# Optimization experiments

Measured on AMD Instinct MI355X. Metric: run time of the kernel, lower is better.

Reference implementation:

```python
import jax, jax.numpy as jnp
import numpy as np


def _lga_pass(x, filters, radius):
    # x: [N, C, H, W]; filters: [N, (2r+1)^2, H, W]
    # out[n,c,h,w] = sum_{i,j in [-r,r]} filters[n,(i+r)*(2r+1)+(j+r),h,w] * x[n,c,h+i,w+j]
    N, C, H, W = x.shape
    k = 2 * radius + 1
    xp = jnp.pad(x, ((0, 0), (0, 0), (radius, radius), (radius, radius)))
    out = jnp.zeros_like(x)
    idx = 0
    for i in range(k):  # fixed small kernel loop (25 taps), accumulates without materializing [N,C,H,W,25]
        for j in range(k):
            out = out + filters[:, idx:idx + 1] * xp[:, :, i:i + H, j:j + W]
            idx += 1
    return out


def setup_inputs() -> dict:
    key = jax.random.key(0)
    k1, k2 = jax.random.split(key)
    input1 = jax.random.normal(k1, (2, 64, 256, 512), dtype=jnp.float32)
    input2 = jax.random.uniform(k2, (2, 25, 256, 512), dtype=jnp.float32)
    return {"input1": input1, "input2": input2, "radius": 2}


def reference(input1, input2, radius):
    # LGA applied twice with the same per-pixel filters (Lga2Function.forward)
    temp = _lga_pass(input1, input2, radius)
    out = _lga_pass(temp, input2, radius)
    return out
```

## Files before the change

### kernel.cpp

```cpp
#include <hip/hip_runtime.h>
#include <hip/hip_fp16.h>


typedef __fp16 h2v __attribute__((ext_vector_type(2)));

#define OH 12
#define OW 60
#define USH 40

__device__ __forceinline__ unsigned pkh(float a, float b) {
    union { h2v h; unsigned u; } c;
    c.h = __builtin_amdgcn_cvt_pkrtz(a, b);
    return c.u;
}

#define M(ac, fv, xv, sf, sx) \
    asm("v_fma_mix_f32 %0, %1, %2, %0 op_sel:[" #sf "," #sx ",0] op_sel_hi:[1,1,0]" \
        : "+v"(ac) : "v"(fv), "v"(xv));

#define ROWM(T, w0, w1, w2, w3) \
  M(a0,frA[T+0],w0,0,0) M(a1,frA[T+0],w0,1,1) M(a2,frB[T+0],w1,0,0) M(a3,frB[T+0],w1,1,1) \
  M(a0,frA[T+1],w0,0,1) M(a1,frA[T+1],w1,1,0) M(a2,frB[T+1],w1,0,1) M(a3,frB[T+1],w2,1,0) \
  M(a0,frA[T+2],w1,0,0) M(a1,frA[T+2],w1,1,1) M(a2,frB[T+2],w2,0,0) M(a3,frB[T+2],w2,1,1) \
  M(a0,frA[T+3],w1,0,1) M(a1,frA[T+3],w2,1,0) M(a2,frB[T+3],w2,0,1) M(a3,frB[T+3],w3,1,0) \
  M(a0,frA[T+4],w2,0,0) M(a1,frA[T+4],w2,1,1) M(a2,frB[T+4],w3,0,0) M(a3,frB[T+4],w3,1,1)

#define LBAR() { asm volatile("s_waitcnt lgkmcnt(0)" ::: "memory"); \
                 __builtin_amdgcn_s_barrier(); asm volatile("" ::: "memory"); }

__global__ __launch_bounds__(256)
void lga2_fused(const float* __restrict__ x, const float* __restrict__ f,
                float* __restrict__ out, int N, int C, int H, int W, int CPB) {
    const int tid = threadIdx.x;
    const int r = tid >> 4;
    const int s = tid & 15;
    const int oh0 = blockIdx.y * OH;
    const int ow0 = blockIdx.x * OW;
    const int CG = C / CPB;
    const int n  = blockIdx.z / CG;
    const int c0 = (blockIdx.z % CG) * CPB;
    const int HW = H * W;

    __shared__ unsigned sxU[2][20 * USH];
    __shared__ unsigned stU[16 * USH];

    if (tid < 32) {
        int row = tid & 15;
        stU[row * USH + ((tid & 16) ? 33 : 0)] = 0u;
    }

    const int gh_f = oh0 - 2 + r;
    const int gwb  = ow0 - 2 + 4 * s;
    const bool rowok = (gh_f >= 0) && (gh_f < H);
    const bool p0ok = rowok && (gwb >= 0) && (gwb + 1 < W);
    const bool p1ok = rowok && (gwb + 3 < W);
    const float* fb = f + (size_t)(n * 25) * HW + (size_t)(rowok ? gh_f : 0) * W;

    unsigned frA[25], frB[25];
    #pragma unroll
    for (int t = 0; t < 25; ++t) {
        float2 v01 = p0ok ? *(const float2*)(fb + (size_t)t * HW + gwb)
                          : make_float2(0.f, 0.f);
        float2 v23 = p1ok ? *(const float2*)(fb + (size_t)t * HW + gwb + 2)
                          : make_float2(0.f, 0.f);
        frA[t] = pkh(v01.x, v01.y);
        frB[t] = pkh(v23.x, v23.y);
        if ((t % 5) == 4) __builtin_amdgcn_sched_barrier(0);
    }
    #pragma unroll
    for (int t = 0; t < 25; ++t)
        asm volatile("" : "+v"(frA[t]), "+v"(frB[t]));

    const int i1 = tid + 256;
    const bool has1 = (tid < 340 - 256);
    const int row0 = tid / 17, v0 = tid - row0 * 17;
    const int row1 = i1 / 17,  v1 = i1 - row1 * 17;
    const int g0h = oh0 - 4 + row0, g0c = ow0 - 4 + 4 * v0;
    const int g1h = oh0 - 4 + row1, g1c = ow0 - 4 + 4 * v1;
    const bool ok0 = (g0h >= 0) && (g0h < H) && (g0c >= 0) && (g0c + 3 < W);
    const bool ok1 = has1 && (g1h >= 0) && (g1h < H) && (g1c >= 0) && (g1c + 3 < W);
    const int off0 = ok0 ? (g0h * W + g0c) : 0;
    const int off1 = ok1 ? (g1h * W + g1c) : 0;
    const int l0u = row0 * USH + 2 * v0;
    const int l1u = row1 * USH + 2 * v1;

    const float4 z4 = make_float4(0.f, 0.f, 0.f, 0.f);
    const float* xc = x + (size_t)(n * C + c0) * HW;

    {
        float4 p = ok0 ? *(const float4*)(xc + off0) : z4;
        *(uint2*)&sxU[0][l0u] = make_uint2(pkh(p.x, p.y), pkh(p.z, p.w));
        if (has1) {
            float4 q = ok1 ? *(const float4*)(xc + off1) : z4;
            *(uint2*)&sxU[0][l1u] = make_uint2(pkh(q.x, q.y), pkh(q.z, q.w));
        }
    }
    __syncthreads();

    const bool prow = (r >= 2) && (r <= 13) && (gh_f < H);
    const int rc = (r < 2) ? 2 : ((r > 13) ? 13 : r);
    float* op = out + ((size_t)(n * C + c0) * H + gh_f) * W + gwb;

    int cur = 0;
    for (int cc = 0; cc < CPB; ++cc) {
        float4 nx0 = z4, nx1 = z4;
        const bool pf = (cc + 1 < CPB);
        if (pf) {
            const float* xn = xc + (size_t)(cc + 1) * HW;
            if (ok0) nx0 = *(const float4*)(xn + off0);
            if (ok1) nx1 = *(const float4*)(xn + off1);
        }

        float a0 = 0.f, a1 = 0.f, a2 = 0.f, a3 = 0.f;
        {
            const unsigned* sxp = sxU[cur];
            #pragma unroll
            for (int i = 0; i < 5; ++i) {
                const int b = (r + i) * USH + 2 * s;
                uint2 lo = *(const uint2*)&sxp[b];
                uint2 hi = *(const uint2*)&sxp[b + 2];
                ROWM(5 * i, lo.x, lo.y, hi.x, hi.y)
            }
        }
        stU[r * USH + 1 + 2 * s] = pkh(a0, a1);
        stU[r * USH + 2 + 2 * s] = pkh(a2, a3);
        LBAR();

        a0 = 0.f; a1 = 0.f; a2 = 0.f; a3 = 0.f;
        #pragma unroll
        for (int i = 0; i < 5; ++i) {
            const int b = (rc - 2 + i) * USH + 2 * s;
            uint2 lo = *(const uint2*)&stU[b];
            uint2 hi = *(const uint2*)&stU[b + 2];
            ROWM(5 * i, lo.x, lo.y, hi.x, hi.y)
        }
        if (prow) {
            if (s >= 1 && gwb + 1 < W)  *(float2*)op       = make_float2(a0, a1);
            if (s <= 14 && gwb + 3 < W) *(float2*)(op + 2) = make_float2(a2, a3);
        }

        if (pf) {
            *(uint2*)&sxU[cur ^ 1][l0u] = make_uint2(pkh(nx0.x, nx0.y), pkh(nx0.z, nx0.w));
            if (has1)
                *(uint2*)&sxU[cur ^ 1][l1u] = make_uint2(pkh(nx1.x, nx1.y), pkh(nx1.z, nx1.w));
        }
        LBAR();
        cur ^= 1;
        op += HW;
    }
}

extern "C" void kernel_launch(void* const* d_in, const int* in_sizes, int n_in,
                              void* d_out, int out_size, void* d_ws, size_t ws_size,
                              hipStream_t stream) {
    const float* x = (const float*)d_in[0];
    const float* f = (const float*)d_in[1];
    float* out = (float*)d_out;

    const int N = 2, C = 64, H = 256, W = 512;
    const int CPB = 16;
    const int CG = C / CPB;

    dim3 grid((W + OW - 1) / OW,
              (H + OH - 1) / OH,
              N * CG);
    lga2_fused<<<grid, 256, 0, stream>>>(x, f, out, N, C, H, W, CPB);
}
```

Before: 79.43 us.

## Double-buffer the intermediate tile and prefetch two channels ahead, one barrier per channel

```diff
diff --git a/kernel.cpp b/kernel.cpp
--- a/kernel.cpp
+++ b/kernel.cpp
@@ -25,8 +25,41 @@
   M(a0,frA[T+3],w1,0,1) M(a1,frA[T+3],w2,1,0) M(a2,frB[T+3],w2,0,1) M(a3,frB[T+3],w3,1,0) \
   M(a0,frA[T+4],w2,0,0) M(a1,frA[T+4],w2,1,1) M(a2,frB[T+4],w3,0,0) M(a3,frB[T+4],w3,1,1)
 
+#define PASS(BUF, ROWBASE) { \
+    a0 = 0.f; a1 = 0.f; a2 = 0.f; a3 = 0.f; \
+    _Pragma("unroll") \
+    for (int i = 0; i < 5; ++i) { \
+        const int b = ((ROWBASE) + i) * USH + 2 * s; \
+        uint2 lo = *(const uint2*)&(BUF)[b]; \
+        uint2 hi = *(const uint2*)&(BUF)[b + 2]; \
+        ROWM(5 * i, lo.x, lo.y, hi.x, hi.y) \
+    } }
+
 #define LBAR() { asm volatile("s_waitcnt lgkmcnt(0)" ::: "memory"); \
                  __builtin_amdgcn_s_barrier(); asm volatile("" ::: "memory"); }
+
+#define BODY(CC, SXR, SXL, STB, NXI0, NXI1, NXL0, NXL1) { \
+    if ((CC) + 2 < CPB) { \
+        if (ok0) NXI0 = *(const float4*)pfp0; \
+        if (ok1) NXI1 = *(const float4*)pfp1; \
+    } \
+    pfp0 += HW; pfp1 += HW; \
+    float a0, a1, a2, a3; \
+    PASS(SXR, r) \
+    (STB)[r * USH + 1 + 2 * s] = pkh(a0, a1); \
+    (STB)[r * USH + 2 + 2 * s] = pkh(a2, a3); \
+    if ((CC) + 1 < CPB) { \
+        *(uint2*)&(SXL)[l0u] = make_uint2(pkh(NXL0.x, NXL0.y), pkh(NXL0.z, NXL0.w)); \
+        if (has1) *(uint2*)&(SXL)[l1u] = make_uint2(pkh(NXL1.x, NXL1.y), pkh(NXL1.z, NXL1.w)); \
+    } \
+    LBAR(); \
+    PASS(STB, rc - 2) \
+    if (prow) { \
+        if (s >= 1 && gwb + 1 < W)  *(float2*)op       = make_float2(a0, a1); \
+        if (s <= 14 && gwb + 3 < W) *(float2*)(op + 2) = make_float2(a2, a3); \
+    } \
+    op += HW; \
+}
 
 __global__ __launch_bounds__(256)
 void lga2_fused(const float* __restrict__ x, const float* __restrict__ f,
@@ -41,12 +74,13 @@
     const int c0 = (blockIdx.z % CG) * CPB;
     const int HW = H * W;
 
-    __shared__ unsigned sxU[2][20 * USH];
-    __shared__ unsigned stU[16 * USH];
+    __shared__ unsigned sx0[20 * USH], sx1[20 * USH];
+    __shared__ unsigned st0[16 * USH], st1[16 * USH];
 
-    if (tid < 32) {
-        int row = tid & 15;
-        stU[row * USH + ((tid & 16) ? 33 : 0)] = 0u;
+    if (tid < 64) {
+        unsigned* stz = (tid < 32) ? st0 : st1;
+        int i = tid & 31, row = i & 15;
+        stz[row * USH + ((i & 16) ? 33 : 0)] = 0u;
     }
 
     const int gh_f = oh0 - 2 + r;
@@ -89,64 +123,28 @@
 
     {
         float4 p = ok0 ? *(const float4*)(xc + off0) : z4;
-        *(uint2*)&sxU[0][l0u] = make_uint2(pkh(p.x, p.y), pkh(p.z, p.w));
+        *(uint2*)&sx0[l0u] = make_uint2(pkh(p.x, p.y), pkh(p.z, p.w));
         if (has1) {
             float4 q = ok1 ? *(const float4*)(xc + off1) : z4;
-            *(uint2*)&sxU[0][l1u] = make_uint2(pkh(q.x, q.y), pkh(q.z, q.w));
+            *(uint2*)&sx0[l1u] = make_uint2(pkh(q.x, q.y), pkh(q.z, q.w));
         }
     }
+    float4 nxA0 = z4, nxA1 = z4, nxB0 = z4, nxB1 = z4;
+    if (CPB > 1) {
+        if (ok0) nxB0 = *(const float4*)(xc + HW + off0);
+        if (ok1) nxB1 = *(const float4*)(xc + HW + off1);
+    }
+    const float* pfp0 = xc + 2 * (size_t)HW + off0;
+    const float* pfp1 = xc + 2 * (size_t)HW + off1;
     __syncthreads();
 
     const bool prow = (r >= 2) && (r <= 13) && (gh_f < H);
     const int rc = (r < 2) ? 2 : ((r > 13) ? 13 : r);
     float* op = out + ((size_t)(n * C + c0) * H + gh_f) * W + gwb;
 
-    int cur = 0;
-    for (int cc = 0; cc < CPB; ++cc) {
-        float4 nx0 = z4, nx1 = z4;
-        const bool pf = (cc + 1 < CPB);
-        if (pf) {
-            const float* xn = xc + (size_t)(cc + 1) * HW;
-            if (ok0) nx0 = *(const float4*)(xn + off0);
-            if (ok1) nx1 = *(const float4*)(xn + off1);
-        }
-
-        float a0 = 0.f, a1 = 0.f, a2 = 0.f, a3 = 0.f;
-        {
-            const unsigned* sxp = sxU[cur];
-            #pragma unroll
-            for (int i = 0; i < 5; ++i) {
-                const int b = (r + i) * USH + 2 * s;
-                uint2 lo = *(const uint2*)&sxp[b];
-                uint2 hi = *(const uint2*)&sxp[b + 2];
-                ROWM(5 * i, lo.x, lo.y, hi.x, hi.y)
-            }
-        }
-        stU[r * USH + 1 + 2 * s] = pkh(a0, a1);
-        stU[r * USH + 2 + 2 * s] = pkh(a2, a3);
-        LBAR();
-
-        a0 = 0.f; a1 = 0.f; a2 = 0.f; a3 = 0.f;
-        #pragma unroll
-        for (int i = 0; i < 5; ++i) {
-            const int b = (rc - 2 + i) * USH + 2 * s;
-            uint2 lo = *(const uint2*)&stU[b];
-            uint2 hi = *(const uint2*)&stU[b + 2];
-            ROWM(5 * i, lo.x, lo.y, hi.x, hi.y)
-        }
-        if (prow) {
-            if (s >= 1 && gwb + 1 < W)  *(float2*)op       = make_float2(a0, a1);
-            if (s <= 14 && gwb + 3 < W) *(float2*)(op + 2) = make_float2(a2, a3);
-        }
-
-        if (pf) {
-            *(uint2*)&sxU[cur ^ 1][l0u] = make_uint2(pkh(nx0.x, nx0.y), pkh(nx0.z, nx0.w));
-            if (has1)
-                *(uint2*)&sxU[cur ^ 1][l1u] = make_uint2(pkh(nx1.x, nx1.y), pkh(nx1.z, nx1.w));
-        }
-        LBAR();
-        cur ^= 1;
-        op += HW;
+    for (int cc = 0; cc < CPB; cc += 2) {
+        BODY(cc,     sx0, sx1, st0, nxA0, nxA1, nxB0, nxB1)
+        BODY(cc + 1, sx1, sx0, st1, nxB0, nxB1, nxA0, nxA1)
     }
 }
 
```

After: 84.12 us. 1.06x slower.
